# Optimization experiments

Measured on AMD Instinct MI355X. Metric: run time of the kernel, lower is better.

## Reference

```python
import jax, jax.numpy as jnp
import numpy as np

DIM = 1024
HEADS = 16
HEAD_DIM = DIM // HEADS
B, S = 4, 4096


def setup_inputs() -> dict:
    key = jax.random.key(0)
    ks = jax.random.split(key, 8)
    sc = 1.0 / np.sqrt(DIM)
    return {
        "x": jax.random.normal(ks[0], (B, S, DIM), dtype=jnp.float32),
        "Wq": jax.random.normal(ks[1], (DIM, DIM), dtype=jnp.float32) * sc,
        "Wk": jax.random.normal(ks[2], (DIM, DIM), dtype=jnp.float32) * sc,
        "Wv": jax.random.normal(ks[3], (DIM, DIM), dtype=jnp.float32) * sc,
        "Wp": jax.random.normal(ks[4], (DIM, DIM), dtype=jnp.float32) * sc,
        "bp": jnp.zeros((DIM,), dtype=jnp.float32),
        "conv_w": jax.random.normal(ks[5], (DIM, 3), dtype=jnp.float32) * (1.0 / np.sqrt(3.0)),
        "conv_b": jnp.zeros((DIM,), dtype=jnp.float32),
    }


def reference(x, Wq, Wk, Wv, Wp, bp, conv_w, conv_b):
    b, s, d = x.shape
    # projections -> [b, h, n, hd] (torch Linear: x @ W.T)
    def split_heads(t):
        return t.reshape(b, s, HEADS, HEAD_DIM).transpose(0, 2, 1, 3)
    q = split_heads(x @ Wq.T)
    k = split_heads(x @ Wk.T)
    v = split_heads(x @ Wv.T)
    # ELU(+1) feature map
    q = jax.nn.elu(q) + 1.0
    k = jax.nn.elu(k) + 1.0
    # global kv-state and k-state
    kv_state = jnp.einsum('bhnd,bhne->bhde', k, v)   # [b,h,hd,hd]
    k_state = k.sum(axis=2)                          # [b,h,hd]
    attn_out = jnp.einsum('bhnd,bhde->bhne', q, kv_state)
    denom = jnp.maximum(jnp.einsum('bhnd,bhd->bhn', q, k_state), 1e-6)[..., None]
    attn_out = (attn_out / denom).transpose(0, 2, 1, 3).reshape(b, s, d)
    # depthwise conv1d, kernel=3, padding=1 (per-channel)
    xp = jnp.pad(x, ((0, 0), (1, 1), (0, 0)))        # [b, s+2, d]
    local = (xp[:, :-2, :] * conv_w[:, 0]
             + xp[:, 1:-1, :] * conv_w[:, 1]
             + xp[:, 2:, :] * conv_w[:, 2]) + conv_b
    return (attn_out + local) @ Wp.T + bp
```

## Files before the change

### kernel.cpp

```cpp
#include <hip/hip_runtime.h>
#include <hip/hip_bf16.h>
#include <stdint.h>

#define DIMN 1024
#define HEADS 16
#define HD 64
#define BATCH 4
#define SEQ 4096
#define M_TOT (BATCH*SEQ)

typedef __attribute__((ext_vector_type(8))) __bf16 bf16x8;
typedef __attribute__((ext_vector_type(4))) __bf16 bf16x4;
typedef __attribute__((ext_vector_type(4))) float f32x4;

__device__ __forceinline__ void gload_lds16(const void* g, void* l) {
  __builtin_amdgcn_global_load_lds(
      (const __attribute__((address_space(1))) void*)(uintptr_t)g,
      (__attribute__((address_space(3))) void*)(uint32_t)(uintptr_t)l,
      16, 0, 0);
}

__device__ __forceinline__ uint32_t swz128(uint32_t off) {
  return off ^ (((off >> 7) & 7) << 4);
}

__device__ __forceinline__ void lfence() { asm volatile("" ::: "memory"); }
__device__ __forceinline__ void barx() { lfence(); __builtin_amdgcn_s_barrier(); lfence(); }

__global__ __launch_bounds__(256) void cast_all_kernel(const float* __restrict__ x,
                                                       const float* __restrict__ wq,
                                                       const float* __restrict__ wk,
                                                       const float* __restrict__ wv,
                                                       const float* __restrict__ wp,
                                                       __bf16* __restrict__ xb,
                                                       __bf16* __restrict__ wqb,
                                                       __bf16* __restrict__ wkb,
                                                       __bf16* __restrict__ wvb,
                                                       __bf16* __restrict__ wpb) {
  int i = blockIdx.x * 256 + threadIdx.x;
  const float* src; __bf16* dst; int j;
  if (i < 4194304)      { src = x;  dst = xb;  j = i; }
  else {
    int t = i - 4194304;
    int w = t >> 18; j = t & 262143;
    if      (w == 0) { src = wq; dst = wqb; }
    else if (w == 1) { src = wk; dst = wkb; }
    else if (w == 2) { src = wv; dst = wvb; }
    else             { src = wp; dst = wpb; }
  }
  f32x4 v = ((const f32x4*)src)[j];
  bf16x4 o;
  o[0] = (__bf16)v[0]; o[1] = (__bf16)v[1]; o[2] = (__bf16)v[2]; o[3] = (__bf16)v[3];
  ((bf16x4*)dst)[j] = o;
}

template <int MODE, int NT>
__global__ __launch_bounds__(512, 2) void gemm256(const __bf16* __restrict__ A,
                                                  const __bf16* __restrict__ Bw,
                                                  void* __restrict__ Cout,
                                                  const float* __restrict__ bias) {
  __shared__ char lds[131072];
  const int KB = DIMN * 2;
  const int NKT = DIMN / 64;
  const int bid = blockIdx.x;
  const int x = bid & 7, jj = bid >> 3;
  const int n_t = jj % NT, m_t = (jj / NT) * 8 + x;
  const int m0 = m_t * 256, n0 = n_t * 256;
  const int tid = threadIdx.x;
  const int lane = tid & 63;
  const int wave = tid >> 6;
  const int wm = wave >> 2;
  const int wn = wave & 3;
  const int r16 = lane & 15, r4 = lane >> 4;

  const uint32_t s_off0 = tid * 16;
  const uint32_t s_off1 = 8192 + tid * 16;
  const uint32_t s_row0 = s_off0 >> 7, s_row1 = s_off1 >> 7;
  const uint32_t s_col0 = (s_off0 ^ ((s_row0 & 7) << 4)) & 127;
  const uint32_t s_col1 = (s_off1 ^ ((s_row1 & 7) << 4)) & 127;

  const char* Ab = (const char*)A + (size_t)m0 * KB;
  const char* Bb = (const char*)Bw + (size_t)n0 * KB;

  auto STAGE = [&](int op, int h, int kt, int b) {
    const char* gb = (op ? Bb : Ab) + (size_t)(h * 128) * KB + kt * 128;
    char* lb = lds + op * 65536 + b * 32768 + h * 16384;
    gload_lds16(gb + s_row0 * KB + s_col0, lb + s_off0);
    gload_lds16(gb + s_row1 * KB + s_col1, lb + s_off1);
  };

  uint32_t axk[2];
#pragma unroll
  for (int k = 0; k < 2; ++k) axk[k] = (uint32_t)(k * 64 + r4 * 16) ^ ((r16 & 7) << 4);

  f32x4 acc[8][4] = {};
  bf16x8 bc[4][2];

  STAGE(1, 0, 0, 0); STAGE(1, 1, 0, 0); STAGE(0, 0, 0, 0); STAGE(0, 1, 0, 0);
  STAGE(1, 0, 1, 1); STAGE(1, 1, 1, 1); STAGE(0, 0, 1, 1);
  asm volatile("s_waitcnt vmcnt(6)" ::: "memory");
  barx();

  for (int kt = 0; kt < NKT; ++kt) {
    const int p = kt & 1;
    const char* abuf = lds + p * 32768;
    const char* bbuf = lds + 65536 + p * 32768;

    {
      bf16x8 af[2][2];
#pragma unroll
      for (int nf = 0; nf < 4; ++nf)
#pragma unroll
        for (int k = 0; k < 2; ++k)
          bc[nf][k] = *(const bf16x8*)(bbuf + (nf >> 1) * 16384 +
                        (((nf & 1) * 64 + wn * 16 + r16) << 7) + axk[k]);
#pragma unroll
      for (int i = 0; i < 2; ++i)
#pragma unroll
        for (int k = 0; k < 2; ++k)
          af[i][k] = *(const bf16x8*)(abuf + ((i * 32 + wm * 16 + r16) << 7) + axk[k]);
      if (kt + 1 < NKT) STAGE(0, 1, kt + 1, (kt + 1) & 1);
      barx();
      __builtin_amdgcn_s_setprio(1);
#pragma unroll
      for (int i = 0; i < 2; ++i)
#pragma unroll
        for (int nf = 0; nf < 4; ++nf)
#pragma unroll
          for (int k = 0; k < 2; ++k)
            acc[i][nf] = __builtin_amdgcn_mfma_f32_16x16x32_bf16(bc[nf][k], af[i][k], acc[i][nf], 0, 0, 0);
      __builtin_amdgcn_s_setprio(0);
      barx();
    }
    {
      bf16x8 af[2][2];
#pragma unroll
      for (int i = 0; i < 2; ++i)
#pragma unroll
        for (int k = 0; k < 2; ++k)
          af[i][k] = *(const bf16x8*)(abuf + (((2 + i) * 32 + wm * 16 + r16) << 7) + axk[k]);
      if (kt + 2 < NKT) STAGE(1, 0, kt + 2, p);
      barx();
      __builtin_amdgcn_s_setprio(1);
#pragma unroll
      for (int i = 0; i < 2; ++i)
#pragma unroll
        for (int nf = 0; nf < 4; ++nf)
#pragma unroll
          for (int k = 0; k < 2; ++k)
            acc[2 + i][nf] = __builtin_amdgcn_mfma_f32_16x16x32_bf16(bc[nf][k], af[i][k], acc[2 + i][nf], 0, 0, 0);
      __builtin_amdgcn_s_setprio(0);
      barx();
    }
    {
      bf16x8 af[2][2];
#pragma unroll
      for (int i = 0; i < 2; ++i)
#pragma unroll
        for (int k = 0; k < 2; ++k)
          af[i][k] = *(const bf16x8*)(abuf + 16384 + ((i * 32 + wm * 16 + r16) << 7) + axk[k]);
      if (kt + 2 < NKT) STAGE(1, 1, kt + 2, p);
      barx();
      __builtin_amdgcn_s_setprio(1);
#pragma unroll
      for (int i = 0; i < 2; ++i)
#pragma unroll
        for (int nf = 0; nf < 4; ++nf)
#pragma unroll
          for (int k = 0; k < 2; ++k)
            acc[4 + i][nf] = __builtin_amdgcn_mfma_f32_16x16x32_bf16(bc[nf][k], af[i][k], acc[4 + i][nf], 0, 0, 0);
      __builtin_amdgcn_s_setprio(0);
      barx();
    }
    {
      bf16x8 af[2][2];
#pragma unroll
      for (int i = 0; i < 2; ++i)
#pragma unroll
        for (int k = 0; k < 2; ++k)
          af[i][k] = *(const bf16x8*)(abuf + 16384 + (((2 + i) * 32 + wm * 16 + r16) << 7) + axk[k]);
      if (kt + 2 < NKT) STAGE(0, 0, kt + 2, p);
      if (kt == NKT - 2) { asm volatile("s_waitcnt vmcnt(0)" ::: "memory"); }
      else if (kt < NKT - 2) { asm volatile("s_waitcnt vmcnt(6)" ::: "memory"); }
      barx();
      __builtin_amdgcn_s_setprio(1);
#pragma unroll
      for (int i = 0; i < 2; ++i)
#pragma unroll
        for (int nf = 0; nf < 4; ++nf)
#pragma unroll
          for (int k = 0; k < 2; ++k)
            acc[6 + i][nf] = __builtin_amdgcn_mfma_f32_16x16x32_bf16(bc[nf][k], af[i][k], acc[6 + i][nf], 0, 0, 0);
      __builtin_amdgcn_s_setprio(0);
      barx();
    }
  }

  const int wsel = n0 >> 10;
  const bool do_elu = (MODE == 3) && (wsel < 2);
#pragma unroll
  for (int mf = 0; mf < 8; ++mf) {
    const int row = m0 + mf * 32 + wm * 16 + r16;
#pragma unroll
    for (int nf = 0; nf < 4; ++nf) {
      const int n = n0 + nf * 64 + wn * 16 + r4 * 4;
      if (MODE == 2) {
        f32x4 bq = *(const f32x4*)(bias + n);
        f32x4 o;
#pragma unroll
        for (int r = 0; r < 4; ++r) o[r] = acc[mf][nf][r] + bq[r];
        *(f32x4*)&((float*)Cout)[(size_t)row * DIMN + n] = o;
      } else {
        bf16x4 o;
#pragma unroll
        for (int r = 0; r < 4; ++r) {
          float v = acc[mf][nf][r];
          if (do_elu) v = (v > 0.f) ? (v + 1.f) : __expf(v);
          o[r] = (__bf16)v;
        }
        int c = n & 1023;
        int h = c >> 6, e2 = c & 63;
        int b = row >> 12, s = row & 4095;
        *(bf16x4*)&((__bf16*)Cout)[(size_t)wsel * 16777216 +
                    ((size_t)((b * HEADS + h) * SEQ + s)) * HD + e2] = o;
      }
    }
  }
}

__global__ __launch_bounds__(256) void kv_state_mfma(const __bf16* __restrict__ kp,
                                                     const __bf16* __restrict__ vb,
                                                     float* __restrict__ kv,
                                                     float* __restrict__ ks) {
  __shared__ __bf16 kt[64][136];
  __shared__ __bf16 vt[80][136];
  const int bid = blockIdx.x;
  const int bh = bid >> 2, nc = bid & 3;
  const int tid = threadIdx.x;
  const int lane = tid & 63;
  const int wave = tid >> 6;
  const int r16 = lane & 15, r4 = lane >> 4;

  for (int i = tid; i < 16 * 136; i += 256) {
    int rr = i / 136;
    vt[64 + rr][i - rr * 136] = (rr == 0) ? (__bf16)1.0f : (__bf16)0.0f;
  }

  const int trow = tid >> 1;
  const int tcol = (tid & 1) * 32;

  f32x4 acc[5] = {};
  bf16x8 kr[4], vr[4];

  size_t gb = ((size_t)bh * SEQ + nc * 1024 + trow) * HD + tcol;
#pragma unroll
  for (int q = 0; q < 4; ++q) {
    kr[q] = *(const bf16x8*)(kp + gb + q * 8);
    vr[q] = *(const bf16x8*)(vb + gb + q * 8);
  }

  for (int t = 0; t < 8; ++t) {
    __syncthreads();
#pragma unroll
    for (int q = 0; q < 4; ++q)
#pragma unroll
      for (int j = 0; j < 8; ++j) {
        kt[tcol + q * 8 + j][trow] = kr[q][j];
        vt[tcol + q * 8 + j][trow] = vr[q][j];
      }
    __syncthreads();
    if (t < 7) {
      size_t gb2 = ((size_t)bh * SEQ + nc * 1024 + (t + 1) * 128 + trow) * HD + tcol;
#pragma unroll
      for (int q = 0; q < 4; ++q) {
        kr[q] = *(const bf16x8*)(kp + gb2 + q * 8);
        vr[q] = *(const bf16x8*)(vb + gb2 + q * 8);
      }
    }
#pragma unroll
    for (int ksl = 0; ksl < 4; ++ksl) {
      bf16x8 af = *(const bf16x8*)&kt[wave * 16 + r16][ksl * 32 + r4 * 8];
#pragma unroll
      for (int eb = 0; eb < 5; ++eb) {
        bf16x8 bf_ = *(const bf16x8*)&vt[eb * 16 + r16][ksl * 32 + r4 * 8];
        acc[eb] = __builtin_amdgcn_mfma_f32_16x16x32_bf16(af, bf_, acc[eb], 0, 0, 0);
      }
    }
  }

#pragma unroll
  for (int eb = 0; eb < 4; ++eb)
#pragma unroll
    for (int r = 0; r < 4; ++r) {
      int d = wave * 16 + r4 * 4 + r;
      atomicAdd(&kv[(size_t)bh * 4096 + d * 64 + eb * 16 + r16], acc[eb][r]);
    }
  if (r16 == 0) {
#pragma unroll
    for (int r = 0; r < 4; ++r)
      atomicAdd(&ks[bh * 64 + wave * 16 + r4 * 4 + r], acc[4][r]);
  }
}

__global__ __launch_bounds__(256) void prep_kv_kernel(const float* __restrict__ kv,
                                                      const float* __restrict__ ks,
                                                      __bf16* __restrict__ kvb) {
  const int bh = blockIdx.x;
  const int tid = threadIdx.x;
  for (int idx = tid; idx < 80 * 64; idx += 256) {
    int e = idx >> 6, d = idx & 63;
    float v;
    if (e < 64)       v = kv[(size_t)bh * 4096 + d * 64 + e];
    else if (e == 64) v = ks[bh * 64 + d];
    else              v = 0.f;
    kvb[(size_t)bh * 5120 + idx] = (__bf16)v;
  }
}

__global__ __launch_bounds__(256) void attn_local_mfma(const __bf16* __restrict__ qp,
                                                       const __bf16* __restrict__ kvb,
                                                       const float* __restrict__ x,
                                                       const float* __restrict__ conv_w,
                                                       const float* __restrict__ conv_b,
                                                       __bf16* __restrict__ y) {
  __shared__ __bf16 qs[128 * 64];
  __shared__ __bf16 bs[80 * 64];
  const int bid = blockIdx.x;
  const int bh = bid >> 5;
  const int chunk = bid & 31;
  const int tid = threadIdx.x;
  const int lane = tid & 63;
  const int wave = tid >> 6;
  const int r16 = lane & 15, r4 = lane >> 4;

  const char* qbase  = (const char*)(qp + ((size_t)bh * SEQ + chunk * 128) * HD);
  const char* kvbase = (const char*)(kvb + (size_t)bh * 5120);
#pragma unroll
  for (int t = 0; t < 4; ++t) {
    int c = t * 4 + wave;
    uint32_t off = c * 1024 + lane * 16;
    gload_lds16(qbase + swz128(off), ((char*)qs) + off);
  }
#pragma unroll
  for (int t = 0; t < 3; ++t) {
    int c = t * 4 + wave;
    if (c < 10) {
      uint32_t off = c * 1024 + lane * 16;
      gload_lds16(kvbase + swz128(off), ((char*)bs) + off);
    }
  }
  __syncthreads();

  f32x4 acc[2][5] = {};
#pragma unroll
  for (int kstep = 0; kstep < 2; ++kstep) {
    bf16x8 af[2], bfr[5];
#pragma unroll
    for (int i = 0; i < 2; ++i) {
      uint32_t off = (wave * 32 + i * 16 + r16) * 128 + kstep * 64 + r4 * 16;
      af[i] = *(const bf16x8*)(((char*)qs) + swz128(off));
    }
#pragma unroll
    for (int j = 0; j < 5; ++j) {
      uint32_t off = (j * 16 + r16) * 128 + kstep * 64 + r4 * 16;
      bfr[j] = *(const bf16x8*)(((char*)bs) + swz128(off));
    }
#pragma unroll
    for (int i = 0; i < 2; ++i)
#pragma unroll
      for (int j = 0; j < 5; ++j)
        acc[i][j] = __builtin_amdgcn_mfma_f32_16x16x32_bf16(af[i], bfr[j], acc[i][j], 0, 0, 0);
  }

  const int b = bh >> 4, h = bh & 15;
  float w0[4], w1[4], w2[4], bb[4];
#pragma unroll
  for (int j = 0; j < 4; ++j) {
    int c = h * HD + j * 16 + r16;
    w0[j] = conv_w[c * 3 + 0]; w1[j] = conv_w[c * 3 + 1]; w2[j] = conv_w[c * 3 + 2];
    bb[j] = conv_b[c];
  }
#pragma unroll
  for (int i = 0; i < 2; ++i) {
#pragma unroll
    for (int r = 0; r < 4; ++r) {
      int s = chunk * 128 + wave * 32 + i * 16 + r4 * 4 + r;
      size_t m = (size_t)b * SEQ + s;
      float den = fmaxf(__shfl(acc[i][4][r], lane & 48), 1e-6f);
      float inv = 1.0f / den;
#pragma unroll
      for (int j = 0; j < 4; ++j) {
        int c = h * HD + j * 16 + r16;
        float xm = x[m * DIMN + c];
        float xl = (s > 0)       ? x[(m - 1) * DIMN + c] : 0.f;
        float xr = (s < SEQ - 1) ? x[(m + 1) * DIMN + c] : 0.f;
        float val = acc[i][j][r] * inv
                  + xl * w0[j] + xm * w1[j] + xr * w2[j] + bb[j];
        y[m * DIMN + c] = (__bf16)val;
      }
    }
  }
}

extern "C" void kernel_launch(void* const* d_in, const int* in_sizes, int n_in,
                              void* d_out, int out_size, void* d_ws, size_t ws_size,
                              hipStream_t stream) {
  const float* x  = (const float*)d_in[0];
  const float* Wq = (const float*)d_in[1];
  const float* Wk = (const float*)d_in[2];
  const float* Wv = (const float*)d_in[3];
  const float* Wp = (const float*)d_in[4];
  const float* bp = (const float*)d_in[5];
  const float* cw = (const float*)d_in[6];
  const float* cb = (const float*)d_in[7];
  float* out = (float*)d_out;

  char* ws = (char*)d_ws;
  const size_t MB = 1024 * 1024;
  __bf16* xb  = (__bf16*)(ws);
  __bf16* y   = xb;
  __bf16* qp  = (__bf16*)(ws + 32 * MB);
  __bf16* kp  = (__bf16*)(ws + 64 * MB);
  __bf16* vb  = (__bf16*)(ws + 96 * MB);
  __bf16* wqb = (__bf16*)(ws + 128 * MB);
  __bf16* wkb = (__bf16*)(ws + 130 * MB);
  __bf16* wvb = (__bf16*)(ws + 132 * MB);
  __bf16* wpb = (__bf16*)(ws + 134 * MB);
  float*  kv  = (float*)(ws + 136 * MB);
  float*  ks  = (float*)(ws + 137 * MB);
  __bf16* kvb = wqb;

  cast_all_kernel<<<20480, 256, 0, stream>>>(x, Wq, Wk, Wv, Wp, xb, wqb, wkb, wvb, wpb);

  gemm256<3, 12><<<768, 512, 0, stream>>>(xb, wqb, qp, nullptr);

  hipMemsetAsync(kv, 0, 64 * 4096 * 4 + 64 * 64 * 4, stream);
  kv_state_mfma<<<256, 256, 0, stream>>>(kp, vb, kv, ks);
  prep_kv_kernel<<<64, 256, 0, stream>>>(kv, ks, kvb);

  attn_local_mfma<<<2048, 256, 0, stream>>>(qp, kvb, x, cw, cb, y);

  gemm256<2, 4><<<256, 512, 0, stream>>>(y, wpb, out, bp);
}
```

Baseline: 241.5 us.

## Fuse fp32-to-bf16 cast of x into the QKV GEMM A-operand load

Drops the separate cast of x to bf16. The QKV GEMM now reads fp32 x straight into registers, converts it, and writes swizzled bf16 into LDS with a new two-half pipeline, while B still uses direct global-to-LDS loads. This removes one write and one reread of a 32MB bf16 copy of x. In exchange the GEMM reads twice the A bytes (fp32) across 12 N-tiles per M row, and the A path costs extra VGPRs and VALU conversion work.

```diff
diff --git a/kernel.cpp b/kernel.cpp
--- a/kernel.cpp
+++ b/kernel.cpp
@@ -27,35 +27,30 @@
 __device__ __forceinline__ void lfence() { asm volatile("" ::: "memory"); }
 __device__ __forceinline__ void barx() { lfence(); __builtin_amdgcn_s_barrier(); lfence(); }
 
-__global__ __launch_bounds__(256) void cast_all_kernel(const float* __restrict__ x,
-                                                       const float* __restrict__ wq,
-                                                       const float* __restrict__ wk,
-                                                       const float* __restrict__ wv,
-                                                       const float* __restrict__ wp,
-                                                       __bf16* __restrict__ xb,
-                                                       __bf16* __restrict__ wqb,
-                                                       __bf16* __restrict__ wkb,
-                                                       __bf16* __restrict__ wvb,
-                                                       __bf16* __restrict__ wpb) {
+__global__ __launch_bounds__(256) void cast_w_kernel(const float* __restrict__ wq,
+                                                     const float* __restrict__ wk,
+                                                     const float* __restrict__ wv,
+                                                     const float* __restrict__ wp,
+                                                     __bf16* __restrict__ wqb,
+                                                     __bf16* __restrict__ wkb,
+                                                     __bf16* __restrict__ wvb,
+                                                     __bf16* __restrict__ wpb) {
   int i = blockIdx.x * 256 + threadIdx.x;
-  const float* src; __bf16* dst; int j;
-  if (i < 4194304)      { src = x;  dst = xb;  j = i; }
-  else {
-    int t = i - 4194304;
-    int w = t >> 18; j = t & 262143;
-    if      (w == 0) { src = wq; dst = wqb; }
-    else if (w == 1) { src = wk; dst = wkb; }
-    else if (w == 2) { src = wv; dst = wvb; }
-    else             { src = wp; dst = wpb; }
-  }
+  int w = i >> 18, j = i & 262143;
+  const float* src; __bf16* dst;
+  if      (w == 0) { src = wq; dst = wqb; }
+  else if (w == 1) { src = wk; dst = wkb; }
+  else if (w == 2) { src = wv; dst = wvb; }
+  else             { src = wp; dst = wpb; }
   f32x4 v = ((const f32x4*)src)[j];
   bf16x4 o;
   o[0] = (__bf16)v[0]; o[1] = (__bf16)v[1]; o[2] = (__bf16)v[2]; o[3] = (__bf16)v[3];
   ((bf16x4*)dst)[j] = o;
 }
 
-template <int MODE, int NT>
+template <int MODE, int NT, bool AF32>
 __global__ __launch_bounds__(512, 2) void gemm256(const __bf16* __restrict__ A,
+                                                  const float* __restrict__ Af,
                                                   const __bf16* __restrict__ Bw,
                                                   void* __restrict__ Cout,
                                                   const float* __restrict__ bias) {
@@ -79,12 +74,11 @@
   const uint32_t s_col0 = (s_off0 ^ ((s_row0 & 7) << 4)) & 127;
   const uint32_t s_col1 = (s_off1 ^ ((s_row1 & 7) << 4)) & 127;
 
-  const char* Ab = (const char*)A + (size_t)m0 * KB;
   const char* Bb = (const char*)Bw + (size_t)n0 * KB;
 
-  auto STAGE = [&](int op, int h, int kt, int b) {
-    const char* gb = (op ? Bb : Ab) + (size_t)(h * 128) * KB + kt * 128;
-    char* lb = lds + op * 65536 + b * 32768 + h * 16384;
+  auto BSTAGE = [&](int h, int kt, int b) {
+    const char* gb = Bb + (size_t)(h * 128) * KB + kt * 128;
+    char* lb = lds + 65536 + b * 32768 + h * 16384;
     gload_lds16(gb + s_row0 * KB + s_col0, lb + s_off0);
     gload_lds16(gb + s_row1 * KB + s_col1, lb + s_off1);
   };
@@ -96,103 +90,205 @@
   f32x4 acc[8][4] = {};
   bf16x8 bc[4][2];
 
-  STAGE(1, 0, 0, 0); STAGE(1, 1, 0, 0); STAGE(0, 0, 0, 0); STAGE(0, 1, 0, 0);
-  STAGE(1, 0, 1, 1); STAGE(1, 1, 1, 1); STAGE(0, 0, 1, 1);
-  asm volatile("s_waitcnt vmcnt(6)" ::: "memory");
-  barx();
-
-  for (int kt = 0; kt < NKT; ++kt) {
-    const int p = kt & 1;
-    const char* abuf = lds + p * 32768;
-    const char* bbuf = lds + 65536 + p * 32768;
-
-    {
-      bf16x8 af[2][2];
-#pragma unroll
-      for (int nf = 0; nf < 4; ++nf)
-#pragma unroll
-        for (int k = 0; k < 2; ++k)
-          bc[nf][k] = *(const bf16x8*)(bbuf + (nf >> 1) * 16384 +
-                        (((nf & 1) * 64 + wn * 16 + r16) << 7) + axk[k]);
-#pragma unroll
-      for (int i = 0; i < 2; ++i)
-#pragma unroll
-        for (int k = 0; k < 2; ++k)
-          af[i][k] = *(const bf16x8*)(abuf + ((i * 32 + wm * 16 + r16) << 7) + axk[k]);
-      if (kt + 1 < NKT) STAGE(0, 1, kt + 1, (kt + 1) & 1);
-      barx();
-      __builtin_amdgcn_s_setprio(1);
-#pragma unroll
-      for (int i = 0; i < 2; ++i)
+  if constexpr (AF32) {
+    const char* Axf = (const char*)Af + (size_t)m0 * 4096;
+    const int a_row = tid >> 4;
+    const uint32_t a_colB = (tid & 15) * 16;
+    const uint32_t c8 = (tid & 15) * 8;
+    const uint32_t axw = c8 ^ ((a_row & 7) << 4);
+
+    f32x4 a0ld[4], a1ld[4];
+
+    auto ALOAD = [&](f32x4 (&dst)[4], int h, int kt) {
+#pragma unroll
+      for (int p = 0; p < 4; ++p)
+        dst[p] = *(const f32x4*)(Axf + (size_t)(h * 128 + p * 32 + a_row) * 4096 +
+                                 kt * 256 + a_colB);
+    };
+    auto AWRITE = [&](f32x4 (&src)[4], int h, int b) {
+      char* base = lds + b * 32768 + h * 16384;
+#pragma unroll
+      for (int p = 0; p < 4; ++p) {
+        bf16x4 o;
+        o[0] = (__bf16)src[p][0]; o[1] = (__bf16)src[p][1];
+        o[2] = (__bf16)src[p][2]; o[3] = (__bf16)src[p][3];
+        *(bf16x4*)(base + ((p * 32 + a_row) << 7) + axw) = o;
+      }
+    };
+
+    ALOAD(a0ld, 0, 0);
+    BSTAGE(0, 0, 0); BSTAGE(1, 0, 0);
+    asm volatile("s_waitcnt vmcnt(4)" ::: "memory");
+    AWRITE(a0ld, 0, 0);
+    ALOAD(a1ld, 1, 0);
+    asm volatile("s_waitcnt vmcnt(4)" ::: "memory");
+    asm volatile("s_waitcnt lgkmcnt(0)" ::: "memory");
+    barx();
+
+    for (int kt = 0; kt < NKT; ++kt) {
+      const int p = kt & 1;
+      const char* abuf = lds + p * 32768;
+      const char* bbuf = lds + 65536 + p * 32768;
+      {
+        bf16x8 af[4][2];
 #pragma unroll
         for (int nf = 0; nf < 4; ++nf)
 #pragma unroll
           for (int k = 0; k < 2; ++k)
-            acc[i][nf] = __builtin_amdgcn_mfma_f32_16x16x32_bf16(bc[nf][k], af[i][k], acc[i][nf], 0, 0, 0);
-      __builtin_amdgcn_s_setprio(0);
-      barx();
-    }
-    {
-      bf16x8 af[2][2];
-#pragma unroll
-      for (int i = 0; i < 2; ++i)
-#pragma unroll
-        for (int k = 0; k < 2; ++k)
-          af[i][k] = *(const bf16x8*)(abuf + (((2 + i) * 32 + wm * 16 + r16) << 7) + axk[k]);
-      if (kt + 2 < NKT) STAGE(1, 0, kt + 2, p);
-      barx();
-      __builtin_amdgcn_s_setprio(1);
-#pragma unroll
-      for (int i = 0; i < 2; ++i)
+            bc[nf][k] = *(const bf16x8*)(bbuf + (nf >> 1) * 16384 +
+                          (((nf & 1) * 64 + wn * 16 + r16) << 7) + axk[k]);
+#pragma unroll
+        for (int mf = 0; mf < 4; ++mf)
+#pragma unroll
+          for (int k = 0; k < 2; ++k)
+            af[mf][k] = *(const bf16x8*)(abuf + ((mf * 32 + wm * 16 + r16) << 7) + axk[k]);
+        if (kt + 1 < NKT) {
+          BSTAGE(0, kt + 1, p ^ 1); BSTAGE(1, kt + 1, p ^ 1);
+          ALOAD(a0ld, 0, kt + 1);
+          asm volatile("s_waitcnt vmcnt(8)" ::: "memory");
+        } else {
+          asm volatile("s_waitcnt vmcnt(0)" ::: "memory");
+        }
+        AWRITE(a1ld, 1, p);
+        asm volatile("s_waitcnt lgkmcnt(0)" ::: "memory");
+        barx();
+        __builtin_amdgcn_s_setprio(1);
+#pragma unroll
+        for (int mf = 0; mf < 4; ++mf)
+#pragma unroll
+          for (int nf = 0; nf < 4; ++nf)
+#pragma unroll
+            for (int k = 0; k < 2; ++k)
+              acc[mf][nf] = __builtin_amdgcn_mfma_f32_16x16x32_bf16(bc[nf][k], af[mf][k], acc[mf][nf], 0, 0, 0);
+        __builtin_amdgcn_s_setprio(0);
+      }
+      {
+        bf16x8 af[4][2];
+#pragma unroll
+        for (int mf = 0; mf < 4; ++mf)
+#pragma unroll
+          for (int k = 0; k < 2; ++k)
+            af[mf][k] = *(const bf16x8*)(abuf + 16384 + ((mf * 32 + wm * 16 + r16) << 7) + axk[k]);
+        if (kt + 1 < NKT) {
+          ALOAD(a1ld, 1, kt + 1);
+          asm volatile("s_waitcnt vmcnt(4)" ::: "memory");
+          AWRITE(a0ld, 0, p ^ 1);
+          asm volatile("s_waitcnt lgkmcnt(0)" ::: "memory");
+        }
+        barx();
+        __builtin_amdgcn_s_setprio(1);
+#pragma unroll
+        for (int mf = 0; mf < 4; ++mf)
+#pragma unroll
+          for (int nf = 0; nf < 4; ++nf)
+#pragma unroll
+            for (int k = 0; k < 2; ++k)
+              acc[4 + mf][nf] = __builtin_amdgcn_mfma_f32_16x16x32_bf16(bc[nf][k], af[mf][k], acc[4 + mf][nf], 0, 0, 0);
+        __builtin_amdgcn_s_setprio(0);
+      }
+    }
+  } else {
+    const char* Ab = (const char*)A + (size_t)m0 * KB;
+    auto STAGE = [&](int op, int h, int kt, int b) {
+      const char* gb = (op ? Bb : Ab) + (size_t)(h * 128) * KB + kt * 128;
+      char* lb = lds + op * 65536 + b * 32768 + h * 16384;
+      gload_lds16(gb + s_row0 * KB + s_col0, lb + s_off0);
+      gload_lds16(gb + s_row1 * KB + s_col1, lb + s_off1);
+    };
+
+    STAGE(1, 0, 0, 0); STAGE(1, 1, 0, 0); STAGE(0, 0, 0, 0); STAGE(0, 1, 0, 0);
+    STAGE(1, 0, 1, 1); STAGE(1, 1, 1, 1); STAGE(0, 0, 1, 1);
+    asm volatile("s_waitcnt vmcnt(6)" ::: "memory");
+    barx();
+
+    for (int kt = 0; kt < NKT; ++kt) {
+      const int p = kt & 1;
+      const char* abuf = lds + p * 32768;
+      const char* bbuf = lds + 65536 + p * 32768;
+      {
+        bf16x8 af[2][2];
 #pragma unroll
         for (int nf = 0; nf < 4; ++nf)
 #pragma unroll
           for (int k = 0; k < 2; ++k)
-            acc[2 + i][nf] = __builtin_amdgcn_mfma_f32_16x16x32_bf16(bc[nf][k], af[i][k], acc[2 + i][nf], 0, 0, 0);
-      __builtin_amdgcn_s_setprio(0);
-      barx();
-    }
-    {
-      bf16x8 af[2][2];
-#pragma unroll
-      for (int i = 0; i < 2; ++i)
-#pragma unroll
-        for (int k = 0; k < 2; ++k)
-          af[i][k] = *(const bf16x8*)(abuf + 16384 + ((i * 32 + wm * 16 + r16) << 7) + axk[k]);
-      if (kt + 2 < NKT) STAGE(1, 1, kt + 2, p);
-      barx();
-      __builtin_amdgcn_s_setprio(1);
-#pragma unroll
-      for (int i = 0; i < 2; ++i)
-#pragma unroll
-        for (int nf = 0; nf < 4; ++nf)
-#pragma unroll
-          for (int k = 0; k < 2; ++k)
-            acc[4 + i][nf] = __builtin_amdgcn_mfma_f32_16x16x32_bf16(bc[nf][k], af[i][k], acc[4 + i][nf], 0, 0, 0);
-      __builtin_amdgcn_s_setprio(0);
-      barx();
-    }
-    {
-      bf16x8 af[2][2];
-#pragma unroll
-      for (int i = 0; i < 2; ++i)
-#pragma unroll
-        for (int k = 0; k < 2; ++k)
-          af[i][k] = *(const bf16x8*)(abuf + 16384 + (((2 + i) * 32 + wm * 16 + r16) << 7) + axk[k]);
-      if (kt + 2 < NKT) STAGE(0, 0, kt + 2, p);
-      if (kt == NKT - 2) { asm volatile("s_waitcnt vmcnt(0)" ::: "memory"); }
-      else if (kt < NKT - 2) { asm volatile("s_waitcnt vmcnt(6)" ::: "memory"); }
-      barx();
-      __builtin_amdgcn_s_setprio(1);
-#pragma unroll
-      for (int i = 0; i < 2; ++i)
-#pragma unroll
-        for (int nf = 0; nf < 4; ++nf)
-#pragma unroll
-          for (int k = 0; k < 2; ++k)
-            acc[6 + i][nf] = __builtin_amdgcn_mfma_f32_16x16x32_bf16(bc[nf][k], af[i][k], acc[6 + i][nf], 0, 0, 0);
-      __builtin_amdgcn_s_setprio(0);
-      barx();
+            bc[nf][k] = *(const bf16x8*)(bbuf + (nf >> 1) * 16384 +
+                          (((nf & 1) * 64 + wn * 16 + r16) << 7) + axk[k]);
+#pragma unroll
+        for (int i = 0; i < 2; ++i)
+#pragma unroll
+          for (int k = 0; k < 2; ++k)
+            af[i][k] = *(const bf16x8*)(abuf + ((i * 32 + wm * 16 + r16) << 7) + axk[k]);
+        if (kt + 1 < NKT) STAGE(0, 1, kt + 1, (kt + 1) & 1);
+        barx();
+        __builtin_amdgcn_s_setprio(1);
+#pragma unroll
+        for (int i = 0; i < 2; ++i)
+#pragma unroll
+          for (int nf = 0; nf < 4; ++nf)
+#pragma unroll
+            for (int k = 0; k < 2; ++k)
+              acc[i][nf] = __builtin_amdgcn_mfma_f32_16x16x32_bf16(bc[nf][k], af[i][k], acc[i][nf], 0, 0, 0);
+        __builtin_amdgcn_s_setprio(0);
+      }
+      {
+        bf16x8 af[2][2];
+#pragma unroll
+        for (int i = 0; i < 2; ++i)
+#pragma unroll
+          for (int k = 0; k < 2; ++k)
+            af[i][k] = *(const bf16x8*)(abuf + (((2 + i) * 32 + wm * 16 + r16) << 7) + axk[k]);
+        if (kt + 2 < NKT) STAGE(1, 0, kt + 2, p);
+        barx();
+        __builtin_amdgcn_s_setprio(1);
+#pragma unroll
+        for (int i = 0; i < 2; ++i)
+#pragma unroll
+          for (int nf = 0; nf < 4; ++nf)
+#pragma unroll
+            for (int k = 0; k < 2; ++k)
+              acc[2 + i][nf] = __builtin_amdgcn_mfma_f32_16x16x32_bf16(bc[nf][k], af[i][k], acc[2 + i][nf], 0, 0, 0);
+        __builtin_amdgcn_s_setprio(0);
+      }
+      {
+        bf16x8 af[2][2];
+#pragma unroll
+        for (int i = 0; i < 2; ++i)
+#pragma unroll
+          for (int k = 0; k < 2; ++k)
+            af[i][k] = *(const bf16x8*)(abuf + 16384 + ((i * 32 + wm * 16 + r16) << 7) + axk[k]);
+        if (kt + 2 < NKT) STAGE(1, 1, kt + 2, p);
+        barx();
+        __builtin_amdgcn_s_setprio(1);
+#pragma unroll
+        for (int i = 0; i < 2; ++i)
+#pragma unroll
+          for (int nf = 0; nf < 4; ++nf)
+#pragma unroll
+            for (int k = 0; k < 2; ++k)
+              acc[4 + i][nf] = __builtin_amdgcn_mfma_f32_16x16x32_bf16(bc[nf][k], af[i][k], acc[4 + i][nf], 0, 0, 0);
+        __builtin_amdgcn_s_setprio(0);
+      }
+      {
+        bf16x8 af[2][2];
+#pragma unroll
+        for (int i = 0; i < 2; ++i)
+#pragma unroll
+          for (int k = 0; k < 2; ++k)
+            af[i][k] = *(const bf16x8*)(abuf + 16384 + (((2 + i) * 32 + wm * 16 + r16) << 7) + axk[k]);
+        if (kt + 2 < NKT) STAGE(0, 0, kt + 2, p);
+        if (kt == NKT - 2) { asm volatile("s_waitcnt vmcnt(0)" ::: "memory"); }
+        else if (kt < NKT - 2) { asm volatile("s_waitcnt vmcnt(6)" ::: "memory"); }
+        barx();
+        __builtin_amdgcn_s_setprio(1);
+#pragma unroll
+        for (int i = 0; i < 2; ++i)
+#pragma unroll
+          for (int nf = 0; nf < 4; ++nf)
+#pragma unroll
+            for (int k = 0; k < 2; ++k)
+              acc[6 + i][nf] = __builtin_amdgcn_mfma_f32_16x16x32_bf16(bc[nf][k], af[i][k], acc[6 + i][nf], 0, 0, 0);
+        __builtin_amdgcn_s_setprio(0);
+      }
     }
   }
 
@@ -417,8 +513,7 @@
 
   char* ws = (char*)d_ws;
   const size_t MB = 1024 * 1024;
-  __bf16* xb  = (__bf16*)(ws);
-  __bf16* y   = xb;
+  __bf16* y   = (__bf16*)(ws);
   __bf16* qp  = (__bf16*)(ws + 32 * MB);
   __bf16* kp  = (__bf16*)(ws + 64 * MB);
   __bf16* vb  = (__bf16*)(ws + 96 * MB);
@@ -430,9 +525,9 @@
   float*  ks  = (float*)(ws + 137 * MB);
   __bf16* kvb = wqb;
 
-  cast_all_kernel<<<20480, 256, 0, stream>>>(x, Wq, Wk, Wv, Wp, xb, wqb, wkb, wvb, wpb);
-
-  gemm256<3, 12><<<768, 512, 0, stream>>>(xb, wqb, qp, nullptr);
+  cast_w_kernel<<<4096, 256, 0, stream>>>(Wq, Wk, Wv, Wp, wqb, wkb, wvb, wpb);
+
+  gemm256<3, 12, true><<<768, 512, 0, stream>>>(nullptr, x, wqb, qp, nullptr);
 
   hipMemsetAsync(kv, 0, 64 * 4096 * 4 + 64 * 64 * 4, stream);
   kv_state_mfma<<<256, 256, 0, stream>>>(kp, vb, kv, ks);
@@ -440,5 +535,5 @@
 
   attn_local_mfma<<<2048, 256, 0, stream>>>(qp, kvb, x, cw, cb, y);
 
-  gemm256<2, 4><<<256, 512, 0, stream>>>(y, wpb, out, bp);
-}
+  gemm256<2, 4, false><<<256, 512, 0, stream>>>(y, nullptr, wpb, out, bp);
+}
```

Result: slower. 247.3 us (+2.4%).
